# Kernel optimization log

Measured on AMD Instinct MI355X. Metric: run time of the kernel, lower is better.

Reference implementation:

```python
import jax, jax.numpy as jnp
import numpy as np

H, HKV, D = 32, 8, 128          # query heads, kv heads, head dim
G = H // HKV                     # GQA group size
PAGE, TOPK = 64, 64              # page size, top-k pages per (b, kv-head)
SCALE = D ** -0.5


def rotate_half(x):
    x1, x2 = x[..., : x.shape[-1] // 2], x[..., x.shape[-1] // 2 :]
    return jnp.concatenate((-x2, x1), axis=-1)


def setup_inputs() -> dict:
    key = jax.random.key(0)
    ks = jax.random.split(key, 8)
    B, Q, HID, S = 4, 1, 4096, 16384
    hidden_states = jax.random.normal(ks[0], (B, Q, HID), jnp.float32)
    # rotary embedding for current decode position S
    inv_freq = 1.0 / (10000.0 ** (np.arange(0, D, 2, dtype=np.float32) / D))
    ang = np.float32(S) * inv_freq
    emb = np.concatenate([ang, ang])  # [D]
    cos = jnp.broadcast_to(jnp.asarray(np.cos(emb))[None, None, :], (B, Q, D)).astype(jnp.float32)
    sin = jnp.broadcast_to(jnp.asarray(np.sin(emb))[None, None, :], (B, Q, D)).astype(jnp.float32)
    k_cache = jax.random.normal(ks[1], (B, HKV, S, D), jnp.float32)
    v_cache = jax.random.normal(ks[2], (B, HKV, S, D), jnp.float32)
    Wq = jax.random.normal(ks[3], (H * D, HID), jnp.float32) * 0.02
    Wk = jax.random.normal(ks[4], (HKV * D, HID), jnp.float32) * 0.02
    Wv = jax.random.normal(ks[5], (HKV * D, HID), jnp.float32) * 0.02
    Wo = jax.random.normal(ks[6], (HID, H * D), jnp.float32) * 0.02
    return dict(hidden_states=hidden_states, cos=cos, sin=sin,
                k_cache=k_cache, v_cache=v_cache, Wq=Wq, Wk=Wk, Wv=Wv, Wo=Wo)


def reference(hidden_states, cos, sin, k_cache, v_cache, Wq, Wk, Wv, Wo):
    B, Q, HID = hidden_states.shape
    S = k_cache.shape[2]
    P = S // PAGE

    # QKV projections (Linear, no bias) -> [B, heads, Q, D]
    q = (hidden_states @ Wq.T).reshape(B, Q, H, D).transpose(0, 2, 1, 3)
    k_new = (hidden_states @ Wk.T).reshape(B, Q, HKV, D).transpose(0, 2, 1, 3)
    v_new = (hidden_states @ Wv.T).reshape(B, Q, HKV, D).transpose(0, 2, 1, 3)

    # RoPE (unsqueeze_dim=1)
    c, s = cos[:, None, :, :], sin[:, None, :, :]
    q = q * c + rotate_half(q) * s
    k_new = k_new * c + rotate_half(k_new) * s

    # merge grouped query heads to kv heads (reduce='mean', merge_mode='kv')
    q_merged = q.reshape(B, HKV, G, Q, D).mean(axis=2)[:, :, 0, :]  # [B, HKV, D]

    # Quest page summaries: per-page elementwise min/max of keys
    Kp = k_cache.reshape(B, HKV, P, PAGE, D)
    Vp = v_cache.reshape(B, HKV, P, PAGE, D)
    kmin = Kp.min(axis=3)  # [B, HKV, P, D]
    kmax = Kp.max(axis=3)
    qm = q_merged[:, :, None, :]
    page_scores = jnp.maximum(qm * kmin, qm * kmax).sum(axis=-1)  # [B, HKV, P]

    # top-k page selection per (batch, kv head), gather selected pages
    _, idx = jax.lax.top_k(page_scores, TOPK)  # [B, HKV, TOPK]
    gidx = idx[:, :, :, None, None]
    K_sel = jnp.take_along_axis(Kp, gidx, axis=2).reshape(B, HKV, TOPK * PAGE, D)
    V_sel = jnp.take_along_axis(Vp, gidx, axis=2).reshape(B, HKV, TOPK * PAGE, D)

    # append current decode token's kv
    K = jnp.concatenate([K_sel, k_new], axis=2)  # [B, HKV, L, D]
    V = jnp.concatenate([V_sel, v_new], axis=2)

    # GQA attention over gathered sparse KV (no mask in quest decode path)
    qg = q.reshape(B, HKV, G, Q, D)
    logits = jnp.einsum('bhgqd,bhld->bhgql', qg, K) * SCALE
    w = jax.nn.softmax(logits.astype(jnp.float32), axis=-1).astype(q.dtype)
    o = jnp.einsum('bhgql,bhld->bhgqd', w, V)              # [B, HKV, G, Q, D]
    o = o.reshape(B, H, Q, D).transpose(0, 2, 1, 3).reshape(B, Q, H * D)
    return o @ Wo.T  # [B, Q, HID]
```

## Files before the change

### kernel.cpp

```cpp
#include <hip/hip_runtime.h>
#include <hip/hip_bf16.h>
#include <math.h>

constexpr int NB    = 4;
constexpr int NHID  = 4096;
constexpr int NHEAD = 32;
constexpr int NKV   = 8;
constexpr int NGQ   = 4;
constexpr int ND    = 128;
constexpr int NS    = 16384;
constexpr int NPG   = 64;
constexpr int NP    = 256;
constexpr int NTOP  = 64;
constexpr int NSPLIT = 32;
constexpr int PPS   = NTOP / NSPLIT;
constexpr float FSCALE = 0.08838834764831845f;

__global__ __launch_bounds__(256) void k_qkv(
    const float* __restrict__ hs, const float* __restrict__ Wq,
    const float* __restrict__ Wk, const float* __restrict__ Wv,
    float* __restrict__ qkv) {
  int row0 = blockIdx.x * 4;
  int t = threadIdx.x;
  const float4* x4 = (const float4*)hs;
  const float4* wr[4];
#pragma unroll
  for (int r = 0; r < 4; r++) {
    int row = row0 + r;
    const float* w;
    if (row < 4096)      w = Wq + (size_t)row * NHID;
    else if (row < 5120) w = Wk + (size_t)(row - 4096) * NHID;
    else                 w = Wv + (size_t)(row - 5120) * NHID;
    wr[r] = (const float4*)w;
  }
  float acc[4][4] = {};
  for (int j = t; j < NHID / 4; j += 256) {
    float4 x0 = x4[j], x1 = x4[1024 + j], x2 = x4[2048 + j], x3 = x4[3072 + j];
#pragma unroll
    for (int r = 0; r < 4; r++) {
      float4 w4 = wr[r][j];
      acc[r][0] += w4.x * x0.x + w4.y * x0.y + w4.z * x0.z + w4.w * x0.w;
      acc[r][1] += w4.x * x1.x + w4.y * x1.y + w4.z * x1.z + w4.w * x1.w;
      acc[r][2] += w4.x * x2.x + w4.y * x2.y + w4.z * x2.z + w4.w * x2.w;
      acc[r][3] += w4.x * x3.x + w4.y * x3.y + w4.z * x3.z + w4.w * x3.w;
    }
  }
  __shared__ float red[4][16];
  int lane = t & 63, wv = t >> 6;
#pragma unroll
  for (int r = 0; r < 4; r++)
#pragma unroll
    for (int b = 0; b < 4; b++) {
      float v = acc[r][b];
      v += __shfl_down(v, 32); v += __shfl_down(v, 16); v += __shfl_down(v, 8);
      v += __shfl_down(v, 4);  v += __shfl_down(v, 2);  v += __shfl_down(v, 1);
      if (lane == 0) red[wv][r * 4 + b] = v;
    }
  __syncthreads();
  if (t < 16) {
    int r = t >> 2, b = t & 3;
    float s = red[0][t] + red[1][t] + red[2][t] + red[3][t];
    qkv[(size_t)b * 6144 + row0 + r] = s;
  }
}

__global__ __launch_bounds__(256) void k_rope_merge(
    const float* __restrict__ qkv, const float* __restrict__ cosp,
    const float* __restrict__ sinp, float* __restrict__ qr,
    float* __restrict__ kn, float* __restrict__ vn, float* __restrict__ qm) {
  int b = blockIdx.x >> 3, kv = blockIdx.x & 7;
  const float* cs = cosp + b * ND;
  const float* sn = sinp + b * ND;
  int t = threadIdx.x;
  int g = t >> 6, i = t & 63;
  __shared__ float sq[4][ND];
  {
    int h = kv * NGQ + g;
    const float* q = qkv + (size_t)b * 6144 + h * ND;
    float x1 = q[i], x2 = q[i + 64];
    float o1 = x1 * cs[i] - x2 * sn[i];
    float o2 = x2 * cs[i + 64] + x1 * sn[i + 64];
    float* dst = qr + ((size_t)b * NHEAD + h) * ND;
    dst[i] = o1; dst[i + 64] = o2;
    sq[g][i] = o1; sq[g][i + 64] = o2;
  }
  if (t < 64) {
    const float* k = qkv + (size_t)b * 6144 + 4096 + kv * ND;
    float x1 = k[t], x2 = k[t + 64];
    float* dst = kn + ((size_t)b * NKV + kv) * ND;
    dst[t] = x1 * cs[t] - x2 * sn[t];
    dst[t + 64] = x2 * cs[t + 64] + x1 * sn[t + 64];
  }
  if (t < 128) {
    vn[((size_t)b * NKV + kv) * ND + t] = qkv[(size_t)b * 6144 + 5120 + kv * ND + t];
  }
  __syncthreads();
  if (t < 128) {
    qm[((size_t)b * NKV + kv) * ND + t] =
        0.25f * (sq[0][t] + sq[1][t] + sq[2][t] + sq[3][t]);
  }
}

__global__ __launch_bounds__(256) void k_pagescore(
    const float* __restrict__ kc, const float* __restrict__ qm,
    float* __restrict__ scores) {
  int bid = blockIdx.x;
  int p = bid & (NP - 1);
  int bh = bid >> 8;
  const float* base = kc + ((size_t)bh * NS + (size_t)p * NPG) * ND;
  int t = threadIdx.x, c = t & 127, hlf = t >> 7;
  float mn = INFINITY, mx = -INFINITY;
  const float* ptr = base + (size_t)hlf * 32 * ND + c;
  for (int r = 0; r < 32; r++) {
    float v = ptr[(size_t)r * ND];
    mn = fminf(mn, v); mx = fmaxf(mx, v);
  }
  __shared__ float smn[256], smx[256], ssc[128];
  smn[t] = mn; smx[t] = mx;
  __syncthreads();
  if (t < 128) {
    float qv = qm[(size_t)bh * ND + t];
    float lo = fminf(smn[t], smn[t + 128]);
    float hi = fmaxf(smx[t], smx[t + 128]);
    ssc[t] = fmaxf(qv * lo, qv * hi);
  }
  __syncthreads();
  if (t < 64) {
    float s = ssc[t] + ssc[t + 64];
    s += __shfl_down(s, 32); s += __shfl_down(s, 16); s += __shfl_down(s, 8);
    s += __shfl_down(s, 4);  s += __shfl_down(s, 2);  s += __shfl_down(s, 1);
    if (t == 0) scores[bid] = s;
  }
}

__global__ __launch_bounds__(256) void k_topk(
    const float* __restrict__ scores, int* __restrict__ sel) {
  int bh = blockIdx.x;
  int t = threadIdx.x;
  __shared__ float s[256];
  s[t] = scores[(size_t)bh * NP + t];
  __syncthreads();
  float mine = s[t];
  int rank = 0;
  for (int j = 0; j < 256; j++) {
    float v = s[j];
    rank += (v > mine) || (v == mine && j < t);
  }
  if (rank < NTOP) sel[(size_t)bh * NTOP + rank] = t;
}

__global__ __launch_bounds__(256) void k_attn_part(
    const float* __restrict__ kc, const float* __restrict__ vc,
    const float* __restrict__ qr, const int* __restrict__ sel,
    float* __restrict__ part_l, float* __restrict__ part_o) {
  int idx = blockIdx.x;
  int sp = idx & (NSPLIT - 1);
  int bh = idx / NSPLIT;
  int b = bh >> 3, kv = bh & 7;
  int t = threadIdx.x;
  int g = t >> 6, lane = t & 63;
  int h = kv * NGQ + g;
  int half = lane >> 5;
  int li = lane & 31;
  const float4* q4 = (const float4*)(qr + ((size_t)b * NHEAD + h) * ND);
  float4 qv = q4[li];
  float lsum = 0.f;
  float4 o = make_float4(0.f, 0.f, 0.f, 0.f);
#pragma unroll
  for (int pi = 0; pi < PPS; pi++) {
    int page = sel[(size_t)bh * NTOP + sp * PPS + pi];
    const float4* Kp = (const float4*)(kc + ((size_t)bh * NS + (size_t)page * NPG) * ND);
    const float4* Vp = (const float4*)(vc + ((size_t)bh * NS + (size_t)page * NPG) * ND);
    for (int r2 = 0; r2 < NPG / 2; r2++) {
      int r = r2 * 2 + half;
      float4 kk = Kp[r * 32 + li];
      float d = kk.x * qv.x + kk.y * qv.y + kk.z * qv.z + kk.w * qv.w;
      d += __shfl_xor(d, 1); d += __shfl_xor(d, 2); d += __shfl_xor(d, 4);
      d += __shfl_xor(d, 8); d += __shfl_xor(d, 16);
      float w = __expf(d * FSCALE);
      lsum += w;
      float4 vv = Vp[r * 32 + li];
      o.x += w * vv.x; o.y += w * vv.y; o.z += w * vv.z; o.w += w * vv.w;
    }
  }
  o.x += __shfl_xor(o.x, 32); o.y += __shfl_xor(o.y, 32);
  o.z += __shfl_xor(o.z, 32); o.w += __shfl_xor(o.w, 32);
  lsum += __shfl_xor(lsum, 32);
  if (half == 0) {
    float4* po = (float4*)(part_o + (((size_t)bh * NGQ + g) * NSPLIT + sp) * ND);
    po[li] = o;
    if (li == 0) part_l[((size_t)bh * NGQ + g) * NSPLIT + sp] = lsum;
  }
}

__global__ __launch_bounds__(64) void k_combine(
    const float* __restrict__ qr, const float* __restrict__ kn,
    const float* __restrict__ vn, const float* __restrict__ part_l,
    const float* __restrict__ part_o, float* __restrict__ attno) {
  int bid = blockIdx.x;
  int b = bid >> 5, h = bid & 31;
  int kv = h >> 2, g = h & 3;
  int lane = threadIdx.x;
  int bh = b * NKV + kv;
  const float2* q2 = (const float2*)(qr + ((size_t)b * NHEAD + h) * ND);
  const float2* k2 = (const float2*)(kn + (size_t)bh * ND);
  float2 qv = q2[lane], kk = k2[lane];
  float d = qv.x * kk.x + qv.y * kk.y;
  d += __shfl_xor(d, 1); d += __shfl_xor(d, 2); d += __shfl_xor(d, 4);
  d += __shfl_xor(d, 8); d += __shfl_xor(d, 16); d += __shfl_xor(d, 32);
  float wn = __expf(d * FSCALE);
  const float2* v2 = (const float2*)(vn + (size_t)bh * ND);
  float2 vv = v2[lane];
  float ox = wn * vv.x, oy = wn * vv.y, lt = wn;
  const float* pl = part_l + ((size_t)bh * NGQ + g) * NSPLIT;
  const float2* po = (const float2*)(part_o + (((size_t)bh * NGQ + g) * NSPLIT) * ND);
  for (int s = 0; s < NSPLIT; s++) {
    lt += pl[s];
    float2 p = po[(size_t)s * 64 + lane];
    ox += p.x; oy += p.y;
  }
  float inv = 1.0f / lt;
  float2* ao = (float2*)(attno + ((size_t)b * NHEAD + h) * ND);
  ao[lane] = make_float2(ox * inv, oy * inv);
}

__global__ __launch_bounds__(256) void k_oproj(
    const float* __restrict__ Wo, const float* __restrict__ x,
    float* __restrict__ out) {
  int row0 = blockIdx.x * 4;
  int t = threadIdx.x;
  const float4* x4 = (const float4*)x;
  float acc[4][4] = {};
  for (int j = t; j < NHID / 4; j += 256) {
    float4 x0 = x4[j], x1 = x4[1024 + j], x2 = x4[2048 + j], x3 = x4[3072 + j];
#pragma unroll
    for (int r = 0; r < 4; r++) {
      float4 w4 = ((const float4*)(Wo + (size_t)(row0 + r) * NHID))[j];
      acc[r][0] += w4.x * x0.x + w4.y * x0.y + w4.z * x0.z + w4.w * x0.w;
      acc[r][1] += w4.x * x1.x + w4.y * x1.y + w4.z * x1.z + w4.w * x1.w;
      acc[r][2] += w4.x * x2.x + w4.y * x2.y + w4.z * x2.z + w4.w * x2.w;
      acc[r][3] += w4.x * x3.x + w4.y * x3.y + w4.z * x3.z + w4.w * x3.w;
    }
  }
  __shared__ float red[4][16];
  int lane = t & 63, wv = t >> 6;
#pragma unroll
  for (int r = 0; r < 4; r++)
#pragma unroll
    for (int b = 0; b < 4; b++) {
      float v = acc[r][b];
      v += __shfl_down(v, 32); v += __shfl_down(v, 16); v += __shfl_down(v, 8);
      v += __shfl_down(v, 4);  v += __shfl_down(v, 2);  v += __shfl_down(v, 1);
      if (lane == 0) red[wv][r * 4 + b] = v;
    }
  __syncthreads();
  if (t < 16) {
    int r = t >> 2, b = t & 3;
    float s = red[0][t] + red[1][t] + red[2][t] + red[3][t];
    out[(size_t)b * NHID + row0 + r] = s;
  }
}

extern "C" void kernel_launch(void* const* d_in, const int* in_sizes, int n_in,
                              void* d_out, int out_size, void* d_ws, size_t ws_size,
                              hipStream_t stream) {
  const float* hs   = (const float*)d_in[0];
  const float* cosp = (const float*)d_in[1];
  const float* sinp = (const float*)d_in[2];
  const float* kc   = (const float*)d_in[3];
  const float* vc   = (const float*)d_in[4];
  const float* Wq   = (const float*)d_in[5];
  const float* Wk   = (const float*)d_in[6];
  const float* Wv   = (const float*)d_in[7];
  const float* Wo   = (const float*)d_in[8];
  float* out = (float*)d_out;

  float* ws = (float*)d_ws;
  float* qkv    = ws;
  float* qr     = ws + 24576;
  float* kn     = ws + 40960;
  float* vn     = ws + 45056;
  float* qm     = ws + 49152;
  float* scores = ws + 53248;
  int*   sel    = (int*)(ws + 61440);
  float* part_l = ws + 63488;
  float* part_o = ws + 67584;
  float* attno  = ws + 591872;

  k_qkv<<<6144 / 4, 256, 0, stream>>>(hs, Wq, Wk, Wv, qkv);
  k_rope_merge<<<NB * NKV, 256, 0, stream>>>(qkv, cosp, sinp, qr, kn, vn, qm);
  k_pagescore<<<NB * NKV * NP, 256, 0, stream>>>(kc, qm, scores);
  k_topk<<<NB * NKV, 256, 0, stream>>>(scores, sel);
  k_attn_part<<<NB * NKV * NSPLIT, 256, 0, stream>>>(kc, vc, qr, sel, part_l, part_o);
  k_combine<<<NB * NHEAD, 64, 0, stream>>>(qr, kn, vn, part_l, part_o, attno);
  k_oproj<<<NHID / 4, 256, 0, stream>>>(Wo, attno, out);
}
```

Baseline: 127.1 us.

## Overlap K-page min/max reduction with QKV projection; fuse rope, scoring and top-k

The per-page K min/max reduction does not depend on the query, so it now runs as extra blocks in the same launch as the QKV GEMV. Both phases are bandwidth-bound reads of the weights and the K cache, and sharing one grid lets them overlap. RoPE, the group-mean merge, page scoring against the stored min/max, and top-k ranking are fused into one kernel per (batch, kv head), which removes two launches. The cost is an extra min/max buffer of about 8 MB in the workspace, and scoring now runs on only 32 blocks instead of 8192.

```diff
diff --git a/kernel.cpp b/kernel.cpp
--- a/kernel.cpp
+++ b/kernel.cpp
@@ -16,64 +16,106 @@
 constexpr int PPS   = NTOP / NSPLIT;
 constexpr float FSCALE = 0.08838834764831845f;
 
-__global__ __launch_bounds__(256) void k_qkv(
+constexpr int QKV_BLOCKS = 6144 / 4;
+constexpr int MM_BLOCKS  = NB * NKV * NP;
+
+__global__ __launch_bounds__(256) void k_qkv_minmax(
     const float* __restrict__ hs, const float* __restrict__ Wq,
     const float* __restrict__ Wk, const float* __restrict__ Wv,
-    float* __restrict__ qkv) {
-  int row0 = blockIdx.x * 4;
+    const float* __restrict__ kc, float* __restrict__ qkv,
+    float* __restrict__ kmm) {
+  int bid = blockIdx.x;
   int t = threadIdx.x;
-  const float4* x4 = (const float4*)hs;
-  const float4* wr[4];
-#pragma unroll
-  for (int r = 0; r < 4; r++) {
-    int row = row0 + r;
-    const float* w;
-    if (row < 4096)      w = Wq + (size_t)row * NHID;
-    else if (row < 5120) w = Wk + (size_t)(row - 4096) * NHID;
-    else                 w = Wv + (size_t)(row - 5120) * NHID;
-    wr[r] = (const float4*)w;
-  }
-  float acc[4][4] = {};
-  for (int j = t; j < NHID / 4; j += 256) {
-    float4 x0 = x4[j], x1 = x4[1024 + j], x2 = x4[2048 + j], x3 = x4[3072 + j];
+  if (bid < QKV_BLOCKS) {
+    int row0 = bid * 4;
+    const float4* x4 = (const float4*)hs;
+    const float4* wr[4];
 #pragma unroll
     for (int r = 0; r < 4; r++) {
-      float4 w4 = wr[r][j];
-      acc[r][0] += w4.x * x0.x + w4.y * x0.y + w4.z * x0.z + w4.w * x0.w;
-      acc[r][1] += w4.x * x1.x + w4.y * x1.y + w4.z * x1.z + w4.w * x1.w;
-      acc[r][2] += w4.x * x2.x + w4.y * x2.y + w4.z * x2.z + w4.w * x2.w;
-      acc[r][3] += w4.x * x3.x + w4.y * x3.y + w4.z * x3.z + w4.w * x3.w;
-    }
-  }
-  __shared__ float red[4][16];
-  int lane = t & 63, wv = t >> 6;
-#pragma unroll
-  for (int r = 0; r < 4; r++)
-#pragma unroll
-    for (int b = 0; b < 4; b++) {
-      float v = acc[r][b];
-      v += __shfl_down(v, 32); v += __shfl_down(v, 16); v += __shfl_down(v, 8);
-      v += __shfl_down(v, 4);  v += __shfl_down(v, 2);  v += __shfl_down(v, 1);
-      if (lane == 0) red[wv][r * 4 + b] = v;
-    }
-  __syncthreads();
-  if (t < 16) {
-    int r = t >> 2, b = t & 3;
-    float s = red[0][t] + red[1][t] + red[2][t] + red[3][t];
-    qkv[(size_t)b * 6144 + row0 + r] = s;
-  }
-}
-
-__global__ __launch_bounds__(256) void k_rope_merge(
+      int row = row0 + r;
+      const float* w;
+      if (row < 4096)      w = Wq + (size_t)row * NHID;
+      else if (row < 5120) w = Wk + (size_t)(row - 4096) * NHID;
+      else                 w = Wv + (size_t)(row - 5120) * NHID;
+      wr[r] = (const float4*)w;
+    }
+    float acc[4][4] = {};
+    for (int j = t; j < NHID / 4; j += 256) {
+      float4 x0 = x4[j], x1 = x4[1024 + j], x2 = x4[2048 + j], x3 = x4[3072 + j];
+#pragma unroll
+      for (int r = 0; r < 4; r++) {
+        float4 w4 = wr[r][j];
+        acc[r][0] += w4.x * x0.x + w4.y * x0.y + w4.z * x0.z + w4.w * x0.w;
+        acc[r][1] += w4.x * x1.x + w4.y * x1.y + w4.z * x1.z + w4.w * x1.w;
+        acc[r][2] += w4.x * x2.x + w4.y * x2.y + w4.z * x2.z + w4.w * x2.w;
+        acc[r][3] += w4.x * x3.x + w4.y * x3.y + w4.z * x3.z + w4.w * x3.w;
+      }
+    }
+    __shared__ float red[4][16];
+    int lane = t & 63, wv = t >> 6;
+#pragma unroll
+    for (int r = 0; r < 4; r++)
+#pragma unroll
+      for (int b = 0; b < 4; b++) {
+        float v = acc[r][b];
+        v += __shfl_down(v, 32); v += __shfl_down(v, 16); v += __shfl_down(v, 8);
+        v += __shfl_down(v, 4);  v += __shfl_down(v, 2);  v += __shfl_down(v, 1);
+        if (lane == 0) red[wv][r * 4 + b] = v;
+      }
+    __syncthreads();
+    if (t < 16) {
+      int r = t >> 2, b = t & 3;
+      float s = red[0][t] + red[1][t] + red[2][t] + red[3][t];
+      qkv[(size_t)b * 6144 + row0 + r] = s;
+    }
+  } else {
+    int pid = bid - QKV_BLOCKS;
+    const float4* Kp = (const float4*)(kc + (size_t)pid * NPG * ND);
+    int c4 = t & 31, rg = t >> 5;
+    float4 mn = make_float4(INFINITY, INFINITY, INFINITY, INFINITY);
+    float4 mx = make_float4(-INFINITY, -INFINITY, -INFINITY, -INFINITY);
+#pragma unroll
+    for (int r = 0; r < 8; r++) {
+      float4 v = Kp[(rg * 8 + r) * 32 + c4];
+      mn.x = fminf(mn.x, v.x); mn.y = fminf(mn.y, v.y);
+      mn.z = fminf(mn.z, v.z); mn.w = fminf(mn.w, v.w);
+      mx.x = fmaxf(mx.x, v.x); mx.y = fmaxf(mx.y, v.y);
+      mx.z = fmaxf(mx.z, v.z); mx.w = fmaxf(mx.w, v.w);
+    }
+    __shared__ float4 smn[8][32], smx[8][32];
+    smn[rg][c4] = mn; smx[rg][c4] = mx;
+    __syncthreads();
+    if (t < 32) {
+      float4 a = smn[0][t], b4 = smx[0][t];
+#pragma unroll
+      for (int r = 1; r < 8; r++) {
+        float4 u = smn[r][t], w = smx[r][t];
+        a.x = fminf(a.x, u.x); a.y = fminf(a.y, u.y);
+        a.z = fminf(a.z, u.z); a.w = fminf(a.w, u.w);
+        b4.x = fmaxf(b4.x, w.x); b4.y = fmaxf(b4.y, w.y);
+        b4.z = fmaxf(b4.z, w.z); b4.w = fmaxf(b4.w, w.w);
+      }
+      float4* dst = (float4*)kmm + (size_t)pid * 64;
+      dst[t] = a;
+      dst[32 + t] = b4;
+    }
+  }
+}
+
+__global__ __launch_bounds__(256) void k_rope_score_topk(
     const float* __restrict__ qkv, const float* __restrict__ cosp,
-    const float* __restrict__ sinp, float* __restrict__ qr,
-    float* __restrict__ kn, float* __restrict__ vn, float* __restrict__ qm) {
-  int b = blockIdx.x >> 3, kv = blockIdx.x & 7;
+    const float* __restrict__ sinp, const float* __restrict__ kmm,
+    float* __restrict__ qr, float* __restrict__ kn, float* __restrict__ vn,
+    int* __restrict__ sel) {
+  int bh = blockIdx.x;
+  int b = bh >> 3, kv = bh & 7;
   const float* cs = cosp + b * ND;
   const float* sn = sinp + b * ND;
   int t = threadIdx.x;
   int g = t >> 6, i = t & 63;
   __shared__ float sq[4][ND];
+  __shared__ __align__(16) float qmS[ND];
+  __shared__ float sc[NP];
   {
     int h = kv * NGQ + g;
     const float* q = qkv + (size_t)b * 6144 + h * ND;
@@ -87,63 +129,42 @@
   if (t < 64) {
     const float* k = qkv + (size_t)b * 6144 + 4096 + kv * ND;
     float x1 = k[t], x2 = k[t + 64];
-    float* dst = kn + ((size_t)b * NKV + kv) * ND;
+    float* dst = kn + (size_t)bh * ND;
     dst[t] = x1 * cs[t] - x2 * sn[t];
     dst[t + 64] = x2 * cs[t + 64] + x1 * sn[t + 64];
   }
   if (t < 128) {
-    vn[((size_t)b * NKV + kv) * ND + t] = qkv[(size_t)b * 6144 + 5120 + kv * ND + t];
+    vn[(size_t)bh * ND + t] = qkv[(size_t)b * 6144 + 5120 + kv * ND + t];
   }
   __syncthreads();
   if (t < 128) {
-    qm[((size_t)b * NKV + kv) * ND + t] =
-        0.25f * (sq[0][t] + sq[1][t] + sq[2][t] + sq[3][t]);
-  }
-}
-
-__global__ __launch_bounds__(256) void k_pagescore(
-    const float* __restrict__ kc, const float* __restrict__ qm,
-    float* __restrict__ scores) {
-  int bid = blockIdx.x;
-  int p = bid & (NP - 1);
-  int bh = bid >> 8;
-  const float* base = kc + ((size_t)bh * NS + (size_t)p * NPG) * ND;
-  int t = threadIdx.x, c = t & 127, hlf = t >> 7;
-  float mn = INFINITY, mx = -INFINITY;
-  const float* ptr = base + (size_t)hlf * 32 * ND + c;
-  for (int r = 0; r < 32; r++) {
-    float v = ptr[(size_t)r * ND];
-    mn = fminf(mn, v); mx = fmaxf(mx, v);
-  }
-  __shared__ float smn[256], smx[256], ssc[128];
-  smn[t] = mn; smx[t] = mx;
+    qmS[t] = 0.25f * (sq[0][t] + sq[1][t] + sq[2][t] + sq[3][t]);
+  }
   __syncthreads();
-  if (t < 128) {
-    float qv = qm[(size_t)bh * ND + t];
-    float lo = fminf(smn[t], smn[t + 128]);
-    float hi = fmaxf(smx[t], smx[t + 128]);
-    ssc[t] = fmaxf(qv * lo, qv * hi);
+#pragma unroll
+  for (int rd = 0; rd < 4; rd++) {
+    int p = (t >> 2) + rd * 64;
+    int q = t & 3;
+    const float4* mm = (const float4*)kmm + ((size_t)bh * NP + p) * 64;
+    float s = 0.f;
+#pragma unroll
+    for (int j = 0; j < 8; j++) {
+      float4 mn = mm[q * 8 + j];
+      float4 mx = mm[32 + q * 8 + j];
+      const float4 qv = *(const float4*)&qmS[q * 32 + j * 4];
+      s += fmaxf(qv.x * mn.x, qv.x * mx.x);
+      s += fmaxf(qv.y * mn.y, qv.y * mx.y);
+      s += fmaxf(qv.z * mn.z, qv.z * mx.z);
+      s += fmaxf(qv.w * mn.w, qv.w * mx.w);
+    }
+    s += __shfl_xor(s, 1); s += __shfl_xor(s, 2);
+    if (q == 0) sc[p] = s;
   }
   __syncthreads();
-  if (t < 64) {
-    float s = ssc[t] + ssc[t + 64];
-    s += __shfl_down(s, 32); s += __shfl_down(s, 16); s += __shfl_down(s, 8);
-    s += __shfl_down(s, 4);  s += __shfl_down(s, 2);  s += __shfl_down(s, 1);
-    if (t == 0) scores[bid] = s;
-  }
-}
-
-__global__ __launch_bounds__(256) void k_topk(
-    const float* __restrict__ scores, int* __restrict__ sel) {
-  int bh = blockIdx.x;
-  int t = threadIdx.x;
-  __shared__ float s[256];
-  s[t] = scores[(size_t)bh * NP + t];
-  __syncthreads();
-  float mine = s[t];
+  float mine = sc[t];
   int rank = 0;
-  for (int j = 0; j < 256; j++) {
-    float v = s[j];
+  for (int j = 0; j < NP; j++) {
+    float v = sc[j];
     rank += (v > mine) || (v == mine && j < t);
   }
   if (rank < NTOP) sel[(size_t)bh * NTOP + rank] = t;
@@ -280,17 +301,14 @@
   float* qr     = ws + 24576;
   float* kn     = ws + 40960;
   float* vn     = ws + 45056;
-  float* qm     = ws + 49152;
-  float* scores = ws + 53248;
-  int*   sel    = (int*)(ws + 61440);
-  float* part_l = ws + 63488;
-  float* part_o = ws + 67584;
-  float* attno  = ws + 591872;
-
-  k_qkv<<<6144 / 4, 256, 0, stream>>>(hs, Wq, Wk, Wv, qkv);
-  k_rope_merge<<<NB * NKV, 256, 0, stream>>>(qkv, cosp, sinp, qr, kn, vn, qm);
-  k_pagescore<<<NB * NKV * NP, 256, 0, stream>>>(kc, qm, scores);
-  k_topk<<<NB * NKV, 256, 0, stream>>>(scores, sel);
+  float* kmm    = ws + 49152;
+  int*   sel    = (int*)(ws + 2146304);
+  float* part_l = ws + 2148352;
+  float* part_o = ws + 2152448;
+  float* attno  = ws + 2676736;
+
+  k_qkv_minmax<<<QKV_BLOCKS + MM_BLOCKS, 256, 0, stream>>>(hs, Wq, Wk, Wv, kc, qkv, kmm);
+  k_rope_score_topk<<<NB * NKV, 256, 0, stream>>>(qkv, cosp, sinp, kmm, qr, kn, vn, sel);
   k_attn_part<<<NB * NKV * NSPLIT, 256, 0, stream>>>(kc, vc, qr, sel, part_l, part_o);
   k_combine<<<NB * NHEAD, 64, 0, stream>>>(qr, kn, vn, part_l, part_o, attno);
   k_oproj<<<NHID / 4, 256, 0, stream>>>(Wo, attno, out);
```

Measured after the change: 130.7 us. 2.8% more time.
